# Kernel optimization log

Measured on AMD Instinct MI355X. Metric: run time of the kernel, lower is better.

Reference implementation:

```python
import jax, jax.numpy as jnp
import numpy as np

S, D, B, N, K = 32, 8, 256, 512, 512


def setup_inputs() -> dict:
    key = jax.random.key(0)
    k1, k2 = jax.random.split(key)
    x = jax.random.normal(k1, (S, D, B, N), dtype=jnp.float32)
    # linear-space accumulators (logspace_accumulators=False); strictly positive
    accumulators = jax.random.uniform(k2, (S, D, N, K), dtype=jnp.float32,
                                      minval=0.1, maxval=1.0)
    return {"x": x, "accumulators": accumulators}


def reference(x, accumulators):
    # log-normalize weights over the num_nodes_in axis (axis=2)
    log_w = jax.nn.log_softmax(jnp.log(accumulators), axis=2)  # (s,d,n,k)
    # logmatmul: out[s,d,b,k] = logsumexp_n( x[s,d,b,n] + log_w[s,d,n,k] )
    # stable form: shift by row/col maxes, do an exp-space batched GEMM, log back.
    x_max = jnp.max(x, axis=-1, keepdims=True)        # (s,d,b,1)
    w_max = jnp.max(log_w, axis=2, keepdims=True)      # (s,d,1,k)
    prod = jnp.einsum('sdbn,sdnk->sdbk',
                      jnp.exp(x - x_max), jnp.exp(log_w - w_max))
    return jnp.log(prod) + x_max + w_max              # (s,d,b,k)
```

## Files before the change

### kernel.cpp

```cpp
#include <hip/hip_runtime.h>
#include <hip/hip_bf16.h>


typedef __attribute__((ext_vector_type(8))) __bf16 bf16x8;
typedef __attribute__((ext_vector_type(4))) float f32x4;
typedef __attribute__((ext_vector_type(8))) unsigned short u16x8;

#define SD_TOT 256
#define MB 256
#define NN 512
#define KK 512

__device__ inline unsigned short bf16rn(float f) {
  unsigned int u = __float_as_uint(f);
  u += 0x7fffu + ((u >> 16) & 1u);
  return (unsigned short)(u >> 16);
}
__device__ inline float bf16tof(unsigned short h) {
  return __uint_as_float(((unsigned int)h) << 16);
}

typedef __attribute__((address_space(1))) const unsigned char gas_byte;
typedef __attribute__((address_space(3))) unsigned char las_byte;
#define GLL16(gp, lp) __builtin_amdgcn_global_load_lds((gas_byte*)(const void*)(gp), (las_byte*)(void*)(lp), 16, 0, 0)

__global__ __launch_bounds__(256) void prep_x(const float* __restrict__ x,
                                              unsigned short* __restrict__ Ehi,
                                              unsigned short* __restrict__ Elo) {
  size_t i = ((size_t)blockIdx.x * 256 + threadIdx.x) * 8;
  float4 v0 = *(const float4*)(x + i);
  float4 v1 = *(const float4*)(x + i + 4);
  float e[8] = {__expf(v0.x), __expf(v0.y), __expf(v0.z), __expf(v0.w),
                __expf(v1.x), __expf(v1.y), __expf(v1.z), __expf(v1.w)};
  u16x8 H, L;
#pragma unroll
  for (int j = 0; j < 8; ++j) {
    unsigned short h = bf16rn(e[j]);
    H[j] = h;
    L[j] = bf16rn(e[j] - bf16tof(h));
  }
  *(u16x8*)(Ehi + i) = H;
  *(u16x8*)(Elo + i) = L;
}

__global__ __launch_bounds__(256) void prep_acc(const float* __restrict__ wacc,
                                                unsigned short* __restrict__ Bthi,
                                                unsigned short* __restrict__ Btlo,
                                                float* __restrict__ logsum) {
  __shared__ unsigned int tile[64 * 129];
  __shared__ float part[128 * 16];
  const int t = threadIdx.x;
  const int sd = blockIdx.x >> 2;
  const int k0 = (blockIdx.x & 3) << 7;
  const float* src = wacc + (size_t)sd * NN * KK + k0;
  float preg[8] = {0.f, 0.f, 0.f, 0.f, 0.f, 0.f, 0.f, 0.f};

  for (int ch = 0; ch < 8; ++ch) {
    const int n0 = ch * 64;
    __syncthreads();
#pragma unroll
    for (int ii = 0; ii < 8; ++ii) {
      int idx = ii * 256 + t;
      int r = idx >> 5;
      int c4 = idx & 31;
      float4 v = *(const float4*)(src + (size_t)(n0 + r) * KK + c4 * 4);
      float vv[4] = {v.x, v.y, v.z, v.w};
#pragma unroll
      for (int j = 0; j < 4; ++j) {
        unsigned int h = bf16rn(vv[j]);
        unsigned int l = bf16rn(vv[j] - bf16tof((unsigned short)h));
        tile[r * 129 + c4 * 4 + j] = h | (l << 16);
      }
    }
    __syncthreads();
#pragma unroll
    for (int ii = 0; ii < 8; ++ii) {
      int k = (t >> 4) + 16 * ii;
      int n4 = (t & 15) * 4;
      unsigned int w0 = tile[(n4 + 0) * 129 + k];
      unsigned int w1 = tile[(n4 + 1) * 129 + k];
      unsigned int w2 = tile[(n4 + 2) * 129 + k];
      unsigned int w3 = tile[(n4 + 3) * 129 + k];
      size_t ob = ((size_t)(sd * KK + k0 + k)) * NN + n0 + n4;
      *(ushort4*)(Bthi + ob) = make_ushort4((unsigned short)(w0 & 0xffffu), (unsigned short)(w1 & 0xffffu),
                                            (unsigned short)(w2 & 0xffffu), (unsigned short)(w3 & 0xffffu));
      *(ushort4*)(Btlo + ob) = make_ushort4((unsigned short)(w0 >> 16), (unsigned short)(w1 >> 16),
                                            (unsigned short)(w2 >> 16), (unsigned short)(w3 >> 16));
      preg[ii] += (bf16tof((unsigned short)(w0 & 0xffffu)) + bf16tof((unsigned short)(w0 >> 16))) +
                  (bf16tof((unsigned short)(w1 & 0xffffu)) + bf16tof((unsigned short)(w1 >> 16))) +
                  (bf16tof((unsigned short)(w2 & 0xffffu)) + bf16tof((unsigned short)(w2 >> 16))) +
                  (bf16tof((unsigned short)(w3 & 0xffffu)) + bf16tof((unsigned short)(w3 >> 16)));
    }
  }
  __syncthreads();
#pragma unroll
  for (int ii = 0; ii < 8; ++ii) {
    int k = (t >> 4) + 16 * ii;
    part[k * 16 + (t & 15)] = preg[ii];
  }
  __syncthreads();
  if (t < 128) {
    float s = 0.f;
#pragma unroll
    for (int g = 0; g < 16; ++g) s += part[t * 16 + g];
    logsum[sd * KK + k0 + t] = __logf(s);
  }
}

__global__ __launch_bounds__(512, 2) void gemm_split(const unsigned short* __restrict__ Ehi,
                                                     const unsigned short* __restrict__ Elo,
                                                     const unsigned short* __restrict__ Bthi,
                                                     const unsigned short* __restrict__ Btlo,
                                                     const float* __restrict__ logsum,
                                                     float* __restrict__ out) {
  __shared__ __align__(16) unsigned short sAhi[256 * 64];
  __shared__ __align__(16) unsigned short sAlo[256 * 64];
  __shared__ __align__(16) unsigned short sBhi[256 * 64];
  __shared__ __align__(16) unsigned short sBlo[256 * 64];

  const int bx = blockIdx.x;
  const int wg = (bx & 7) * 64 + (bx >> 3);
  const int sd = wg >> 1;
  const int nt = wg & 1;
  const int t = threadIdx.x;
  const int lane = t & 63;
  const int w = t >> 6;
  const int wm = w >> 2;
  const int wn = w & 3;

  const unsigned short* aH = Ehi + (size_t)sd * MB * NN;
  const unsigned short* aL = Elo + (size_t)sd * MB * NN;
  const unsigned short* bH = Bthi + (size_t)(sd * KK + nt * 256) * NN;
  const unsigned short* bL = Btlo + (size_t)(sd * KK + nt * 256) * NN;

  f32x4 acc[8][4] = {};

  for (int kt = 0; kt < 8; ++kt) {
    __syncthreads();
    const int kb = kt * 64;
#pragma unroll
    for (int q = 0; q < 4; ++q) {
      int gg = q * 512 + t;
      int row = gg >> 3;
      int c8 = (gg & 7) * 8;
      size_t so = (size_t)row * NN + kb + c8;
      GLL16(aH + so, &sAhi[gg * 8]);
      GLL16(aL + so, &sAlo[gg * 8]);
      GLL16(bH + so, &sBhi[gg * 8]);
      GLL16(bL + so, &sBlo[gg * 8]);
    }
    __syncthreads();
#pragma unroll
    for (int kk = 0; kk < 64; kk += 32) {
      const int fo = kk + (lane >> 4) * 8;
      const int fr = lane & 15;
      bf16x8 bh[4], bl[4];
#pragma unroll
      for (int n = 0; n < 4; ++n) {
        int off = (wn * 64 + n * 16 + fr) * 64 + fo;
        bh[n] = *(const bf16x8*)&sBhi[off];
        bl[n] = *(const bf16x8*)&sBlo[off];
      }
#pragma unroll
      for (int m = 0; m < 8; ++m) {
        int offa = (wm * 128 + m * 16 + fr) * 64 + fo;
        bf16x8 ah = *(const bf16x8*)&sAhi[offa];
        bf16x8 al = *(const bf16x8*)&sAlo[offa];
#pragma unroll
        for (int n = 0; n < 4; ++n) {
          acc[m][n] = __builtin_amdgcn_mfma_f32_16x16x32_bf16(ah, bh[n], acc[m][n], 0, 0, 0);
          acc[m][n] = __builtin_amdgcn_mfma_f32_16x16x32_bf16(ah, bl[n], acc[m][n], 0, 0, 0);
          acc[m][n] = __builtin_amdgcn_mfma_f32_16x16x32_bf16(al, bh[n], acc[m][n], 0, 0, 0);
        }
      }
    }
  }

  const size_t obase = (size_t)sd * MB * KK;
  const int colb = nt * 256 + wn * 64;
  float ls[4];
#pragma unroll
  for (int n = 0; n < 4; ++n) ls[n] = logsum[sd * KK + colb + n * 16 + (lane & 15)];
#pragma unroll
  for (int m = 0; m < 8; ++m) {
    int rowb = wm * 128 + m * 16 + (lane >> 4) * 4;
#pragma unroll
    for (int n = 0; n < 4; ++n) {
      int col = colb + n * 16 + (lane & 15);
      f32x4 v = acc[m][n];
#pragma unroll
      for (int q = 0; q < 4; ++q)
        out[obase + (size_t)(rowb + q) * KK + col] = __logf(v[q]) - ls[n];
    }
  }
}

__global__ __launch_bounds__(256) void fb_gemm(const float* __restrict__ x,
                                               const float* __restrict__ wacc,
                                               float* __restrict__ out) {
  const int bx = blockIdx.x;
  const int sd = bx >> 5;
  const int bt = (bx & 31) >> 3;
  const int kt = bx & 7;
  const int b0 = bt * 64, k0 = kt * 64;
  __shared__ float sA[64 * 33];
  __shared__ float sB[32 * 65];
  __shared__ float sLs[64];
  const int t = threadIdx.x;
  float ca[4][4] = {{0.f}};
  const float* xp = x + (size_t)(sd * MB + b0) * NN;
  const float* ap = wacc + (size_t)sd * NN * KK + k0;

  for (int n0 = 0; n0 < NN; n0 += 32) {
    __syncthreads();
#pragma unroll
    for (int q = 0; q < 8; ++q) {
      int e = q * 256 + t;
      int r = e >> 5, c = e & 31;
      sA[r * 33 + c] = __expf(xp[(size_t)r * NN + n0 + c]);
    }
#pragma unroll
    for (int q = 0; q < 8; ++q) {
      int e = q * 256 + t;
      int r = e >> 6, c = e & 63;
      sB[r * 65 + c] = ap[(size_t)(n0 + r) * KK + c];
    }
    __syncthreads();
    const int tr = (t >> 4) * 4, tc = (t & 15) * 4;
    for (int n = 0; n < 32; ++n) {
      float bv0 = sB[n * 65 + tc], bv1 = sB[n * 65 + tc + 1];
      float bv2 = sB[n * 65 + tc + 2], bv3 = sB[n * 65 + tc + 3];
#pragma unroll
      for (int i = 0; i < 4; ++i) {
        float a = sA[(tr + i) * 33 + n];
        ca[i][0] += a * bv0; ca[i][1] += a * bv1;
        ca[i][2] += a * bv2; ca[i][3] += a * bv3;
      }
    }
  }
  __syncthreads();
  if (t < 64) {
    float s = 0.f;
    for (int n = 0; n < NN; ++n) s += ap[(size_t)n * KK + t];
    sLs[t] = __logf(s);
  }
  __syncthreads();
  const int tr = (t >> 4) * 4, tc = (t & 15) * 4;
#pragma unroll
  for (int i = 0; i < 4; ++i)
#pragma unroll
    for (int j2 = 0; j2 < 4; ++j2)
      out[(size_t)(sd * MB + b0 + tr + i) * KK + k0 + tc + j2] = __logf(ca[i][j2]) - sLs[tc + j2];
}

extern "C" void kernel_launch(void* const* d_in, const int* in_sizes, int n_in,
                              void* d_out, int out_size, void* d_ws, size_t ws_size,
                              hipStream_t stream) {
  const float* x = (const float*)d_in[0];
  const float* wacc = (const float*)d_in[1];
  float* out = (float*)d_out;

  const size_t E_ELEMS = (size_t)SD_TOT * MB * NN;
  const size_t B_ELEMS = (size_t)SD_TOT * KK * NN;
  const size_t NEED = 2 * E_ELEMS * 2 + 2 * B_ELEMS * 2 + (size_t)SD_TOT * KK * 4;

  if (ws_size >= NEED) {
    unsigned short* Ehi = (unsigned short*)d_ws;
    unsigned short* Elo = Ehi + E_ELEMS;
    unsigned short* Bthi = (unsigned short*)((char*)d_ws + 2 * E_ELEMS * 2);
    unsigned short* Btlo = Bthi + B_ELEMS;
    float* logsum = (float*)((char*)d_ws + 2 * E_ELEMS * 2 + 2 * B_ELEMS * 2);

    prep_x<<<dim3(16384), dim3(256), 0, stream>>>(x, Ehi, Elo);
    prep_acc<<<dim3(1024), dim3(256), 0, stream>>>(wacc, Bthi, Btlo, logsum);
    gemm_split<<<dim3(512), dim3(512), 0, stream>>>(Ehi, Elo, Bthi, Btlo, logsum, out);
  } else {
    fb_gemm<<<dim3(8192), dim3(256), 0, stream>>>(x, wacc, out);
  }
}
```

Baseline: 699.4 us.

## Fuse x exponentiation and bf16 hi/lo split into the GEMM, drop prep_x

```diff
diff --git a/kernel.cpp b/kernel.cpp
--- a/kernel.cpp
+++ b/kernel.cpp
@@ -10,6 +10,7 @@
 #define MB 256
 #define NN 512
 #define KK 512
+#define B_ELEMS ((size_t)SD_TOT * KK * NN)
 
 __device__ inline unsigned short bf16rn(float f) {
   unsigned int u = __float_as_uint(f);
@@ -24,63 +25,44 @@
 typedef __attribute__((address_space(3))) unsigned char las_byte;
 #define GLL16(gp, lp) __builtin_amdgcn_global_load_lds((gas_byte*)(const void*)(gp), (las_byte*)(void*)(lp), 16, 0, 0)
 
-__global__ __launch_bounds__(256) void prep_x(const float* __restrict__ x,
-                                              unsigned short* __restrict__ Ehi,
-                                              unsigned short* __restrict__ Elo) {
-  size_t i = ((size_t)blockIdx.x * 256 + threadIdx.x) * 8;
-  float4 v0 = *(const float4*)(x + i);
-  float4 v1 = *(const float4*)(x + i + 4);
-  float e[8] = {__expf(v0.x), __expf(v0.y), __expf(v0.z), __expf(v0.w),
-                __expf(v1.x), __expf(v1.y), __expf(v1.z), __expf(v1.w)};
-  u16x8 H, L;
-#pragma unroll
-  for (int j = 0; j < 8; ++j) {
-    unsigned short h = bf16rn(e[j]);
-    H[j] = h;
-    L[j] = bf16rn(e[j] - bf16tof(h));
-  }
-  *(u16x8*)(Ehi + i) = H;
-  *(u16x8*)(Elo + i) = L;
-}
-
 __global__ __launch_bounds__(256) void prep_acc(const float* __restrict__ wacc,
                                                 unsigned short* __restrict__ Bthi,
                                                 unsigned short* __restrict__ Btlo,
                                                 float* __restrict__ logsum) {
-  __shared__ unsigned int tile[64 * 129];
-  __shared__ float part[128 * 16];
+  __shared__ unsigned int tile[64 * 65];
+  __shared__ float part[64 * 16];
   const int t = threadIdx.x;
-  const int sd = blockIdx.x >> 2;
-  const int k0 = (blockIdx.x & 3) << 7;
+  const int sd = blockIdx.x >> 3;
+  const int k0 = (blockIdx.x & 7) << 6;
   const float* src = wacc + (size_t)sd * NN * KK + k0;
-  float preg[8] = {0.f, 0.f, 0.f, 0.f, 0.f, 0.f, 0.f, 0.f};
+  float preg[4] = {0.f, 0.f, 0.f, 0.f};
 
   for (int ch = 0; ch < 8; ++ch) {
     const int n0 = ch * 64;
     __syncthreads();
 #pragma unroll
-    for (int ii = 0; ii < 8; ++ii) {
+    for (int ii = 0; ii < 4; ++ii) {
       int idx = ii * 256 + t;
-      int r = idx >> 5;
-      int c4 = idx & 31;
+      int r = idx >> 4;
+      int c4 = idx & 15;
       float4 v = *(const float4*)(src + (size_t)(n0 + r) * KK + c4 * 4);
       float vv[4] = {v.x, v.y, v.z, v.w};
 #pragma unroll
       for (int j = 0; j < 4; ++j) {
         unsigned int h = bf16rn(vv[j]);
         unsigned int l = bf16rn(vv[j] - bf16tof((unsigned short)h));
-        tile[r * 129 + c4 * 4 + j] = h | (l << 16);
-      }
-    }
-    __syncthreads();
-#pragma unroll
-    for (int ii = 0; ii < 8; ++ii) {
+        tile[r * 65 + c4 * 4 + j] = h | (l << 16);
+      }
+    }
+    __syncthreads();
+#pragma unroll
+    for (int ii = 0; ii < 4; ++ii) {
       int k = (t >> 4) + 16 * ii;
       int n4 = (t & 15) * 4;
-      unsigned int w0 = tile[(n4 + 0) * 129 + k];
-      unsigned int w1 = tile[(n4 + 1) * 129 + k];
-      unsigned int w2 = tile[(n4 + 2) * 129 + k];
-      unsigned int w3 = tile[(n4 + 3) * 129 + k];
+      unsigned int w0 = tile[(n4 + 0) * 65 + k];
+      unsigned int w1 = tile[(n4 + 1) * 65 + k];
+      unsigned int w2 = tile[(n4 + 2) * 65 + k];
+      unsigned int w3 = tile[(n4 + 3) * 65 + k];
       size_t ob = ((size_t)(sd * KK + k0 + k)) * NN + n0 + n4;
       *(ushort4*)(Bthi + ob) = make_ushort4((unsigned short)(w0 & 0xffffu), (unsigned short)(w1 & 0xffffu),
                                             (unsigned short)(w2 & 0xffffu), (unsigned short)(w3 & 0xffffu));
@@ -94,12 +76,12 @@
   }
   __syncthreads();
 #pragma unroll
-  for (int ii = 0; ii < 8; ++ii) {
+  for (int ii = 0; ii < 4; ++ii) {
     int k = (t >> 4) + 16 * ii;
     part[k * 16 + (t & 15)] = preg[ii];
   }
   __syncthreads();
-  if (t < 128) {
+  if (t < 64) {
     float s = 0.f;
 #pragma unroll
     for (int g = 0; g < 16; ++g) s += part[t * 16 + g];
@@ -107,16 +89,12 @@
   }
 }
 
-__global__ __launch_bounds__(512, 2) void gemm_split(const unsigned short* __restrict__ Ehi,
-                                                     const unsigned short* __restrict__ Elo,
-                                                     const unsigned short* __restrict__ Bthi,
-                                                     const unsigned short* __restrict__ Btlo,
-                                                     const float* __restrict__ logsum,
-                                                     float* __restrict__ out) {
-  __shared__ __align__(16) unsigned short sAhi[256 * 64];
-  __shared__ __align__(16) unsigned short sAlo[256 * 64];
-  __shared__ __align__(16) unsigned short sBhi[256 * 64];
-  __shared__ __align__(16) unsigned short sBlo[256 * 64];
+__global__ __launch_bounds__(512) void gemm_fused(const float* __restrict__ x,
+                                                  const unsigned short* __restrict__ Bthi,
+                                                  const float* __restrict__ logsum,
+                                                  float* __restrict__ out) {
+  __shared__ __align__(16) unsigned char sA[65536];
+  __shared__ __align__(16) unsigned char sB[65536];
 
   const int bx = blockIdx.x;
   const int wg = (bx & 7) * 64 + (bx >> 3);
@@ -124,48 +102,81 @@
   const int nt = wg & 1;
   const int t = threadIdx.x;
   const int lane = t & 63;
+  const int fr = lane & 15;
+  const int fq = lane >> 4;
   const int w = t >> 6;
   const int wm = w >> 2;
   const int wn = w & 3;
 
-  const unsigned short* aH = Ehi + (size_t)sd * MB * NN;
-  const unsigned short* aL = Elo + (size_t)sd * MB * NN;
-  const unsigned short* bH = Bthi + (size_t)(sd * KK + nt * 256) * NN;
-  const unsigned short* bL = Btlo + (size_t)(sd * KK + nt * 256) * NN;
+  const float* xp = x + (size_t)sd * MB * NN;
+  const int base_col = sd * KK + nt * 256;
 
   f32x4 acc[8][4] = {};
 
+  const int arow = t >> 1;
+  const int nl0 = (t & 1) * 32;
+
   for (int kt = 0; kt < 8; ++kt) {
-    __syncthreads();
-    const int kb = kt * 64;
+    const int n0 = kt * 64;
+    __syncthreads();
+    const float* ap = xp + (size_t)arow * NN + n0 + nl0;
+    float e[32];
+#pragma unroll
+    for (int q = 0; q < 8; ++q) {
+      float4 v = *(const float4*)(ap + q * 4);
+      e[q * 4 + 0] = __expf(v.x); e[q * 4 + 1] = __expf(v.y);
+      e[q * 4 + 2] = __expf(v.z); e[q * 4 + 3] = __expf(v.w);
+    }
+    unsigned short hi[32], lo[32];
+#pragma unroll
+    for (int j = 0; j < 32; ++j) {
+      hi[j] = bf16rn(e[j]);
+      lo[j] = bf16rn(e[j] - bf16tof(hi[j]));
+    }
 #pragma unroll
     for (int q = 0; q < 4; ++q) {
-      int gg = q * 512 + t;
-      int row = gg >> 3;
-      int c8 = (gg & 7) * 8;
-      size_t so = (size_t)row * NN + kb + c8;
-      GLL16(aH + so, &sAhi[gg * 8]);
-      GLL16(aL + so, &sAlo[gg * 8]);
-      GLL16(bH + so, &sBhi[gg * 8]);
-      GLL16(bL + so, &sBlo[gg * 8]);
-    }
-    __syncthreads();
-#pragma unroll
-    for (int kk = 0; kk < 64; kk += 32) {
-      const int fo = kk + (lane >> 4) * 8;
-      const int fr = lane & 15;
+      int L = (nl0 >> 3) + q;
+      int G = L ^ (arow & 15);
+      u16x8 v;
+#pragma unroll
+      for (int j = 0; j < 8; ++j) v[j] = hi[q * 8 + j];
+      *(u16x8*)(sA + arow * 256 + G * 16) = v;
+      int L2 = 8 + (nl0 >> 3) + q;
+      int G2 = L2 ^ (arow & 15);
+      u16x8 v2;
+#pragma unroll
+      for (int j = 0; j < 8; ++j) v2[j] = lo[q * 8 + j];
+      *(u16x8*)(sA + arow * 256 + G2 * 16) = v2;
+    }
+#pragma unroll
+    for (int q = 0; q < 8; ++q) {
+      int S = q * 512 + t;
+      int kcol = S >> 4;
+      int G = S & 15;
+      int L = G ^ (kcol & 15);
+      int p = L >> 3;
+      int nl = (L & 7) * 8;
+      const unsigned short* srcp = Bthi + (size_t)p * B_ELEMS +
+                                   (size_t)(base_col + kcol) * NN + n0 + nl;
+      GLL16(srcp, sB + (size_t)S * 16);
+    }
+    __syncthreads();
+#pragma unroll
+    for (int kk = 0; kk < 2; ++kk) {
       bf16x8 bh[4], bl[4];
 #pragma unroll
       for (int n = 0; n < 4; ++n) {
-        int off = (wn * 64 + n * 16 + fr) * 64 + fo;
-        bh[n] = *(const bf16x8*)&sBhi[off];
-        bl[n] = *(const bf16x8*)&sBlo[off];
+        int C = wn * 64 + n * 16 + fr;
+        int Lh = kk * 4 + fq;
+        bh[n] = *(const bf16x8*)(sB + C * 256 + ((Lh) ^ (C & 15)) * 16);
+        bl[n] = *(const bf16x8*)(sB + C * 256 + ((Lh + 8) ^ (C & 15)) * 16);
       }
 #pragma unroll
       for (int m = 0; m < 8; ++m) {
-        int offa = (wm * 128 + m * 16 + fr) * 64 + fo;
-        bf16x8 ah = *(const bf16x8*)&sAhi[offa];
-        bf16x8 al = *(const bf16x8*)&sAlo[offa];
+        int R = wm * 128 + m * 16 + fr;
+        int Lh = kk * 4 + fq;
+        bf16x8 ah = *(const bf16x8*)(sA + R * 256 + ((Lh) ^ (R & 15)) * 16);
+        bf16x8 al = *(const bf16x8*)(sA + R * 256 + ((Lh + 8) ^ (R & 15)) * 16);
 #pragma unroll
         for (int n = 0; n < 4; ++n) {
           acc[m][n] = __builtin_amdgcn_mfma_f32_16x16x32_bf16(ah, bh[n], acc[m][n], 0, 0, 0);
@@ -180,13 +191,13 @@
   const int colb = nt * 256 + wn * 64;
   float ls[4];
 #pragma unroll
-  for (int n = 0; n < 4; ++n) ls[n] = logsum[sd * KK + colb + n * 16 + (lane & 15)];
+  for (int n = 0; n < 4; ++n) ls[n] = logsum[sd * KK + colb + n * 16 + fr];
 #pragma unroll
   for (int m = 0; m < 8; ++m) {
-    int rowb = wm * 128 + m * 16 + (lane >> 4) * 4;
+    int rowb = wm * 128 + m * 16 + fq * 4;
 #pragma unroll
     for (int n = 0; n < 4; ++n) {
-      int col = colb + n * 16 + (lane & 15);
+      int col = colb + n * 16 + fr;
       f32x4 v = acc[m][n];
 #pragma unroll
       for (int q = 0; q < 4; ++q)
@@ -260,20 +271,15 @@
   const float* wacc = (const float*)d_in[1];
   float* out = (float*)d_out;
 
-  const size_t E_ELEMS = (size_t)SD_TOT * MB * NN;
-  const size_t B_ELEMS = (size_t)SD_TOT * KK * NN;
-  const size_t NEED = 2 * E_ELEMS * 2 + 2 * B_ELEMS * 2 + (size_t)SD_TOT * KK * 4;
+  const size_t NEED = 2 * B_ELEMS * 2 + (size_t)SD_TOT * KK * 4;
 
   if (ws_size >= NEED) {
-    unsigned short* Ehi = (unsigned short*)d_ws;
-    unsigned short* Elo = Ehi + E_ELEMS;
-    unsigned short* Bthi = (unsigned short*)((char*)d_ws + 2 * E_ELEMS * 2);
+    unsigned short* Bthi = (unsigned short*)d_ws;
     unsigned short* Btlo = Bthi + B_ELEMS;
-    float* logsum = (float*)((char*)d_ws + 2 * E_ELEMS * 2 + 2 * B_ELEMS * 2);
-
-    prep_x<<<dim3(16384), dim3(256), 0, stream>>>(x, Ehi, Elo);
-    prep_acc<<<dim3(1024), dim3(256), 0, stream>>>(wacc, Bthi, Btlo, logsum);
-    gemm_split<<<dim3(512), dim3(512), 0, stream>>>(Ehi, Elo, Bthi, Btlo, logsum, out);
+    float* logsum = (float*)((char*)d_ws + 2 * B_ELEMS * 2);
+
+    prep_acc<<<dim3(2048), dim3(256), 0, stream>>>(wacc, Bthi, Btlo, logsum);
+    gemm_fused<<<dim3(512), dim3(512), 0, stream>>>(x, Bthi, logsum, out);
   } else {
     fb_gemm<<<dim3(8192), dim3(256), 0, stream>>>(x, wacc, out);
   }
```

New measurement: 630.0 us. 9.9% less time.
